# Optimization experiments

Measured on AMD Instinct MI355X. Metric: run time of the kernel, lower is better.

## Reference

```python
import jax, jax.numpy as jnp
import numpy as np
from jax import lax

# ---- model dims (match init_kwargs) ----
D = 2048        # hidden_size
HD = 128        # head_dim
HQ = 16         # num_q_heads (= expanded_num_heads)
HK = 8          # num_k_heads = num_v_heads
CONV = 4        # conv_size
CHUNK = 64      # chunk_size
NUM_ITER = 30   # chebyshev iterations
RIDGE = 0.02
EPS = 1e-6


def setup_inputs() -> dict:
    key = jax.random.key(0)
    ks = jax.random.split(key, 20)
    s = 0.02
    inp = {}
    inp['hidden_states'] = jax.random.normal(ks[0], (1, 1024, D), jnp.float32)
    inp['Wq'] = jax.random.normal(ks[1], (D, HQ * HD), jnp.float32) * s
    inp['Wk'] = jax.random.normal(ks[2], (D, HK * HD), jnp.float32) * s
    inp['Wv'] = jax.random.normal(ks[3], (D, HK * HD), jnp.float32) * s
    inp['conv_q'] = jax.random.normal(ks[4], (HQ * HD, CONV), jnp.float32) * 0.3
    inp['conv_k'] = jax.random.normal(ks[5], (HK * HD, CONV), jnp.float32) * 0.3
    inp['conv_v'] = jax.random.normal(ks[6], (HK * HD, CONV), jnp.float32) * 0.3
    inp['Wa'] = jax.random.normal(ks[7], (D, HQ), jnp.float32) * s
    # A_log = log(Uniform(0,16)) as in torch init
    inp['A_log'] = jnp.log(jax.random.uniform(ks[8], (HQ,), jnp.float32, 1e-3, 16.0))
    # dt_bias = inverse-softplus of dt ~ LogUniform(1e-3, 1e-1)
    dt = jnp.exp(jax.random.uniform(ks[9], (HQ,), jnp.float32) * (np.log(0.1) - np.log(0.001)) + np.log(0.001))
    dt = jnp.clip(dt, 1e-4, None)
    inp['dt_bias'] = dt + jnp.log(-jnp.expm1(-dt))
    inp['Wb'] = jax.random.normal(ks[10], (D, HQ), jnp.float32) * s
    inp['bb'] = jnp.zeros((HQ,), jnp.float32)
    inp['Walpha'] = jax.random.normal(ks[11], (D, HQ), jnp.float32) * s
    inp['balpha'] = jnp.zeros((HQ,), jnp.float32)
    inp['Wg'] = jax.random.normal(ks[12], (D, HQ * HD), jnp.float32) * s
    inp['norm_w'] = jnp.ones((HD,), jnp.float32)
    inp['Wo'] = jax.random.normal(ks[13], (HQ * HD, D), jnp.float32) * s
    return inp


def short_conv(x, w):
    # causal depthwise conv1d (kernel=CONV) + silu; x:[B,L,C], w:[C,K]
    K = w.shape[1]
    L = x.shape[1]
    xp = jnp.pad(x, ((0, 0), (K - 1, 0), (0, 0)))
    y = sum(xp[:, j:j + L, :] * w[:, j] for j in range(K))
    return jax.nn.silu(y)


def cheb_solve(A, b, lmin, lmax, num_iter):
    # Chebyshev semi-iteration for SPD A x = b, eigenvalue bounds [lmin, lmax].
    # A, b: [..., d, d]; lmin scalar; lmax: [..., 1, 1]
    theta = (lmax + lmin) / 2.0
    delta = (lmax - lmin) / 2.0
    sigma1 = theta / delta
    x = jnp.zeros_like(b)
    r = b
    rho = 1.0 / sigma1
    dvec = r / theta
    def body(carry, _):
        x, r, dvec, rho = carry
        x = x + dvec
        r = r - jnp.einsum('...de,...ef->...df', A, dvec)
        rho_n = 1.0 / (2.0 * sigma1 - rho)
        dvec = rho_n * rho * dvec + (2.0 * rho_n / delta) * r
        return (x, r, dvec, rho_n), None
    (x, _, _, _), _ = lax.scan(body, (x, r, dvec, rho), None, length=num_iter)
    return x


def reference(hidden_states, Wq, Wk, Wv, conv_q, conv_k, conv_v, Wa, A_log, dt_bias,
              Wb, bb, Walpha, balpha, Wg, norm_w, Wo):
    x = hidden_states
    B, L, _ = x.shape
    H, Hk, d, C = HQ, HK, HD, CHUNK
    Nc = L // C

    # projections + short causal convs with silu
    q = short_conv(x @ Wq, conv_q).reshape(B, L, H, d) * (d ** -0.5)  # gla rescale
    k = short_conv(x @ Wk, conv_k).reshape(B, L, Hk, d)
    v = short_conv(x @ Wv, conv_v).reshape(B, L, Hk, d)
    grp = H // Hk
    k = jnp.repeat(k, grp, axis=2)  # GQA expand: (h g) ordering
    v = jnp.repeat(v, grp, axis=2)

    # gates
    glog = -jnp.exp(A_log) * jax.nn.softplus(x @ Wa + dt_bias)   # [B,L,H], log forgetting gate <= 0
    beta = jax.nn.sigmoid(x @ Wb + bb)                           # [B,L,H]
    alpha = jax.nn.sigmoid(x @ Walpha + balpha)                  # [B,L,H]

    # chunk: [B,H,Nc,C,...]
    def ch(t):
        return t.reshape(B, Nc, C, H, -1).transpose(0, 3, 1, 2, 4)
    qc, kc, vc = ch(q), ch(k), ch(v)
    glc = glog.reshape(B, Nc, C, H).transpose(0, 3, 1, 2)   # [B,H,Nc,C]
    bc = beta.reshape(B, Nc, C, H).transpose(0, 3, 1, 2)

    cs = jnp.cumsum(glc, axis=-1)         # inclusive cumulative log-decay within chunk
    G = cs[..., -1]                        # total chunk decay [B,H,Nc]
    w_end = jnp.exp(G[..., None] - cs) * bc
    dHn = jnp.einsum('bhnc,bhncd,bhnce->bhnde', w_end, kc, kc)  # gram increment (forgetting_gate_kk)
    dBn = jnp.einsum('bhnc,bhncd,bhnce->bhnde', w_end, kc, vc)  # kv increment
    dg = jnp.exp(G)

    # inter-chunk state recurrence (scan over chunks)
    def step(carry, inp):
        Hs, Bs = carry
        g_n, dH_n, dB_n = inp
        out = (Hs, Bs)  # state at chunk START
        Hs = g_n[..., None, None] * Hs + dH_n
        Bs = g_n[..., None, None] * Bs + dB_n
        return (Hs, Bs), out
    init = (jnp.zeros((B, H, d, d), x.dtype), jnp.zeros((B, H, d, d), x.dtype))
    inputs = (dg.transpose(2, 0, 1), dHn.transpose(2, 0, 1, 3, 4), dBn.transpose(2, 0, 1, 3, 4))
    _, (H0, B0) = lax.scan(step, init, inputs)  # [Nc,B,H,d,d]

    # ridge-regularized Kalman solve per chunk via Chebyshev
    A = H0 + RIDGE * jnp.eye(d, dtype=x.dtype)
    lmax = jnp.trace(A, axis1=-2, axis2=-1)[..., None, None]  # trace >= lambda_max for SPD
    X = cheb_solve(A, B0, RIDGE, lmax, NUM_ITER)              # [Nc,B,H,d,d]
    Xc = X.transpose(1, 2, 0, 3, 4)                           # [B,H,Nc,d,d]

    # inter-chunk readout (through solved state)
    o_inter = jnp.exp(cs)[..., None] * jnp.einsum('bhncd,bhnde->bhnce', qc, Xc)
    # intra-chunk causal gated attention
    diff = cs[..., :, None] - cs[..., None, :]                # [B,H,Nc,C,C]
    mask = jnp.tril(jnp.ones((C, C), bool))
    dmat = jnp.exp(jnp.where(mask, diff, -1e30))
    scores = jnp.einsum('bhncd,bhnjd->bhncj', qc, kc) * dmat * bc[..., None, :]
    o_intra = jnp.einsum('bhncj,bhnjd->bhncd', scores, vc)

    o = (o_inter + o_intra).transpose(0, 2, 3, 1, 4).reshape(B, L, H, d)
    o = o + alpha[..., None] * v   # alpha connection (residual value path)

    # gated RMSNorm + output projection
    g_out = (x @ Wg).reshape(B, L, H, d)
    o = o * lax.rsqrt(jnp.mean(o * o, axis=-1, keepdims=True) + EPS) * norm_w
    o = o * jax.nn.silu(g_out)
    return o.reshape(B, L, H * d) @ Wo
```

## Files before the change

### kernel.cpp

```cpp
#include <hip/hip_runtime.h>
#include <math.h>


#define LSEQ 1024
#define DM   2048
#define NHQ  16
#define NHK  8
#define HDIM 128
#define NCH  16
#define CSZ  64

typedef __attribute__((ext_vector_type(8))) short short8;
typedef __attribute__((ext_vector_type(4))) float floatx4;

__device__ __forceinline__ unsigned short f2bf(float f) {
  unsigned int u = __float_as_uint(f);
  u += 0x7fffu + ((u >> 16) & 1u);
  return (unsigned short)(u >> 16);
}
__device__ __forceinline__ float bf2f(unsigned short u) {
  return __uint_as_float(((unsigned int)u) << 16);
}

__device__ __forceinline__ void gload16(const unsigned short* g,
                                        unsigned short* l) {
  __builtin_amdgcn_global_load_lds(
      (const __attribute__((address_space(1))) unsigned int*)g,
      (__attribute__((address_space(3))) unsigned int*)l, 16, 0, 0);
}

__device__ __forceinline__ void tcast_fat(
    const float* __restrict__ W, unsigned short* __restrict__ Wt,
    int K, int N, int bn, int bk, int tid, float* __restrict__ t) {
  int k0 = bk * 128, n0 = bn * 64;
#pragma unroll
  for (int i = 0; i < 8; ++i) {
    int u = tid + i * 256;
    int r = u >> 4, c4 = u & 15;
    float4 v = *(const float4*)(W + (size_t)(k0 + r) * N + n0 + c4 * 4);
    float* dst = t + r * 65 + c4 * 4;
    dst[0] = v.x; dst[1] = v.y; dst[2] = v.z; dst[3] = v.w;
  }
  __syncthreads();
#pragma unroll
  for (int i = 0; i < 4; ++i) {
    int u2 = tid + i * 256;
    int klow = u2 & 7, nlow = (u2 >> 3) & 7;
    int khigh = (u2 >> 6) & 1, nhigh = (u2 >> 7) & 7;
    int k8 = (klow + khigh * 8) * 8;
    int nn = nlow + nhigh * 8;
    unsigned short o8[8];
#pragma unroll
    for (int j = 0; j < 8; ++j) o8[j] = f2bf(t[(k8 + j) * 65 + nn]);
    *(uint4*)(Wt + (size_t)(n0 + nn) * K + k0 + k8) = *(uint4*)o8;
  }
}

__global__ __launch_bounds__(256) void prep_kernel(
    const float* __restrict__ x, const float* __restrict__ Wq,
    const float* __restrict__ Wk, const float* __restrict__ Wv,
    const float* __restrict__ Wg, unsigned short* __restrict__ xb16,
    unsigned short* __restrict__ WtAll,
    const float* __restrict__ Wa, const float* __restrict__ Wbeta,
    const float* __restrict__ Wal, const float* __restrict__ A_log,
    const float* __restrict__ dtb, const float* __restrict__ bbv,
    const float* __restrict__ balv, float* __restrict__ glog,
    float* __restrict__ beta, float* __restrict__ alpha) {
  __shared__ float smem[128 * 65];
  int b = blockIdx.x, tid = threadIdx.x;
  if (b < 1024) {
    float* xr = smem;
    float* part = smem + 2048;
    int ts = b;
    for (int i = tid; i < 512; i += 256)
      ((float4*)xr)[i] = ((const float4*)(x + (size_t)ts * 2048))[i];
    __syncthreads();
    int o = tid >> 2, p = tid & 3;
    float s = 0.f;
    if (o < 48) {
      const float* W = (o < 16) ? Wa : (o < 32) ? Wbeta : Wal;
      int h = o & 15;
      int k0 = p * 512;
      for (int k = k0; k < k0 + 512; ++k) s = fmaf(xr[k], W[k * 16 + h], s);
    }
    part[tid] = s;
    __syncthreads();
    if (o < 48 && p == 0) {
      float dot = part[tid] + part[tid + 1] + part[tid + 2] + part[tid + 3];
      int h = o & 15;
      if (o < 16) {
        float za = dot + dtb[h];
        float sp = fmaxf(za, 0.f) + log1pf(expf(-fabsf(za)));
        glog[ts * 16 + h] = -expf(A_log[h]) * sp;
      } else if (o < 32) {
        beta[ts * 16 + h] = 1.f / (1.f + expf(-(dot + bbv[h])));
      } else {
        alpha[ts * 16 + h] = 1.f / (1.f + expf(-(dot + balv[h])));
      }
    }
  } else if (b < 2560) {
    int r = b - 1024;
    if (r < 512) {
      tcast_fat(Wq, WtAll, 2048, 2048, r & 31, r >> 5, tid, smem);
    } else if (r < 768) {
      int q = r - 512;
      tcast_fat(Wk, WtAll + (size_t)2048 * 2048, 2048, 1024, q & 15, q >> 4,
                tid, smem);
    } else if (r < 1024) {
      int q = r - 768;
      tcast_fat(Wv, WtAll + (size_t)3072 * 2048, 2048, 1024, q & 15, q >> 4,
                tid, smem);
    } else {
      int q = r - 1024;
      tcast_fat(Wg, WtAll + (size_t)4096 * 2048, 2048, 2048, q & 31, q >> 5,
                tid, smem);
    }
  } else {
    int i0 = (b - 2560) * 1024 + tid;
#pragma unroll
    for (int i = 0; i < 4; ++i) {
      int idx = i0 + i * 256;
      float4 v = ((const float4*)x)[idx];
      ushort4 u;
      u.x = f2bf(v.x); u.y = f2bf(v.y); u.z = f2bf(v.z); u.w = f2bf(v.w);
      ((ushort4*)xb16)[idx] = u;
    }
  }
}

template <int BN>
__global__ __launch_bounds__(256) void gemm_lds(
    const unsigned short* __restrict__ A, const unsigned short* __restrict__ Bt,
    float* __restrict__ C, int M, int N, int K) {
  __shared__ unsigned short As[128 * 64];
  __shared__ unsigned short Bs[BN * 64];
  constexpr int NT = BN / 32;
  constexpr int BCH = BN / 32;
  int tid = threadIdx.x;
  int wave = tid >> 6, lane = tid & 63;
  int ln = lane & 15, hi = lane >> 4;
  int wm = wave & 1, wn = wave >> 1;
  int m0 = blockIdx.y * 128, n0 = blockIdx.x * BN;
  int lrow = lane >> 3, lcol = (lane & 7) * 8;

  floatx4 acc[4][NT];
#pragma unroll
  for (int mt = 0; mt < 4; ++mt)
#pragma unroll
    for (int nt = 0; nt < NT; ++nt) acc[mt][nt] = (floatx4)(0.f);

  for (int k0 = 0; k0 < K; k0 += 64) {
#pragma unroll
    for (int i = 0; i < 4; ++i) {
      int c = wave * 4 + i;
      gload16(A + (size_t)(m0 + c * 8 + lrow) * K + k0 + lcol, As + c * 512);
    }
#pragma unroll
    for (int i = 0; i < BCH; ++i) {
      int c = wave * BCH + i;
      gload16(Bt + (size_t)(n0 + c * 8 + lrow) * K + k0 + lcol, Bs + c * 512);
    }
    __syncthreads();
#pragma unroll
    for (int kb = 0; kb < 2; ++kb) {
      short8 a[4], b[NT];
#pragma unroll
      for (int mt = 0; mt < 4; ++mt)
        a[mt] = *(const short8*)(As + (wm * 64 + mt * 16 + ln) * 64 +
                                 kb * 32 + hi * 8);
#pragma unroll
      for (int nt = 0; nt < NT; ++nt)
        b[nt] = *(const short8*)(Bs + (wn * (BN / 2) + nt * 16 + ln) * 64 +
                                 kb * 32 + hi * 8);
#pragma unroll
      for (int mt = 0; mt < 4; ++mt)
#pragma unroll
        for (int nt = 0; nt < NT; ++nt)
          acc[mt][nt] = __builtin_amdgcn_mfma_f32_16x16x32_bf16(
              a[mt], b[nt], acc[mt][nt], 0, 0, 0);
    }
    __syncthreads();
  }
#pragma unroll
  for (int mt = 0; mt < 4; ++mt)
#pragma unroll
    for (int nt = 0; nt < NT; ++nt) {
      int col = n0 + wn * (BN / 2) + nt * 16 + ln;
      int rowb = m0 + wm * 64 + mt * 16 + hi * 4;
#pragma unroll
      for (int r = 0; r < 4; ++r)
        C[(size_t)(rowb + r) * N + col] = acc[mt][nt][r];
    }
}

__device__ __forceinline__ float conv_core(
    const float* __restrict__ xin, const float* __restrict__ w,
    int idx, int instride, int nch, float scale) {
  int t = idx / nch, ch = idx - t * nch;
  float acc = 0.f;
#pragma unroll
  for (int j = 0; j < 4; ++j) {
    int tt = t + j - 3;
    float xv = (tt >= 0) ? xin[(size_t)tt * instride + ch] : 0.f;
    acc = fmaf(xv, w[ch * 4 + j], acc);
  }
  return acc / (1.f + expf(-acc)) * scale;
}

__global__ __launch_bounds__(256) void conv_all(
    const float* __restrict__ xall, const float* __restrict__ convq,
    const float* __restrict__ convk, const float* __restrict__ convv,
    unsigned short* __restrict__ qs16, float* __restrict__ ks2,
    unsigned short* __restrict__ ks16, float* __restrict__ vs2,
    const float* __restrict__ glog, const float* __restrict__ beta,
    float* __restrict__ cs, float* __restrict__ wend) {
  int b = blockIdx.x, tid = threadIdx.x;
  if (b < 8192) {
    int idx = b * 256 + tid;
    qs16[idx] = f2bf(conv_core(xall, convq, idx, 6144, 2048,
                               0.08838834764831845f));
  } else if (b < 12288) {
    int idx = (b - 8192) * 256 + tid;
    float v = conv_core(xall + 2048, convk, idx, 6144, 1024, 1.0f);
    ks2[idx] = v;
    ks16[idx] = f2bf(v);
  } else if (b < 16384) {
    int idx = (b - 12288) * 256 + tid;
    vs2[idx] = conv_core(xall + 3072, convv, idx, 6144, 1024, 1.0f);
  } else {
    int idx = tid;
    int n = idx & 15;
    float acc = 0.f;
    for (int c = 0; c < CSZ; ++c) {
      acc += glog[(n * CSZ + c) * NHQ + (idx >> 4)];
      cs[idx * CSZ + c] = acc;
    }
    float G = acc;
    for (int c = 0; c < CSZ; ++c) {
      wend[idx * CSZ + c] =
          expf(G - cs[idx * CSZ + c]) * beta[(n * CSZ + c) * NHQ + (idx >> 4)];
    }
  }
}

__global__ __launch_bounds__(256) void dhb_kernel(
    const float* __restrict__ ks, const float* __restrict__ vs,
    const float* __restrict__ wend, float* __restrict__ dH,
    float* __restrict__ dB, unsigned short* __restrict__ vT16) {
  __shared__ uint4 smem4[4096];
  int bid = blockIdx.x;
  int tid = threadIdx.x;

  if (bid >= 256) {
    float* t = (float*)smem4;
    int b = bid - 256;
    size_t gbase = ((size_t)(b >> 3)) * 65536 + ((size_t)(b & 7)) * 128;
#pragma unroll
    for (int g = 0; g < 8; ++g) {
      int i = tid + g * 256;
      int c = i >> 5, e4 = i & 31;
      float4 v = *(const float4*)(vs + gbase + (size_t)c * 1024 + e4 * 4);
      t[c * 132 + e4 * 4 + 0] = v.x;
      t[c * 132 + e4 * 4 + 1] = v.y;
      t[c * 132 + e4 * 4 + 2] = v.z;
      t[c * 132 + e4 * 4 + 3] = v.w;
    }
    __syncthreads();
    int e = tid >> 1, half = tid & 1;
    size_t obase = ((size_t)b << 13) + (size_t)e * 64 + half * 32;
#pragma unroll
    for (int cc = 0; cc < 8; ++cc) {
      int c0 = half * 32 + cc * 4;
      ushort4 u;
      u.x = f2bf(t[(c0 + 0) * 132 + e]);
      u.y = f2bf(t[(c0 + 1) * 132 + e]);
      u.z = f2bf(t[(c0 + 2) * 132 + e]);
      u.w = f2bf(t[(c0 + 3) * 132 + e]);
      *(ushort4*)(vT16 + obase + cc * 4) = u;
    }
    return;
  }

  unsigned short (*skF)[8192] = (unsigned short (*)[8192])smem4;
  unsigned short (*svF)[8192] =
      (unsigned short (*)[8192])((unsigned short*)smem4 + 16384);
  int h = bid >> 4, n = bid & 15;
  int hk = h >> 1;

#pragma unroll
  for (int p = 0; p < 4; ++p) {
    int t2 = tid + p * 256;
    int c0 = (t2 >> 7) << 3;
    int e = t2 & 127;
    int base = ((e >> 4) * 2 + (c0 >> 5)) * 512 +
               ((c0 & 31) >> 3) * 128 + (e & 15) * 8;
    unsigned short kh[8], kl[8], vh[8], vl[8];
#pragma unroll
    for (int j = 0; j < 8; ++j) {
      int c = c0 + j;
      float s = sqrtf(wend[bid * 64 + c]);
      size_t g = (size_t)(n * 64 + c) * 1024 + hk * 128 + e;
      float kf = s * ks[g];
      float vf = s * vs[g];
      unsigned short khh = f2bf(kf);
      kh[j] = khh; kl[j] = f2bf(kf - bf2f(khh));
      unsigned short vhh = f2bf(vf);
      vh[j] = vhh; vl[j] = f2bf(vf - bf2f(vhh));
    }
    *(uint4*)(&skF[0][base]) = *(uint4*)kh;
    *(uint4*)(&skF[1][base]) = *(uint4*)kl;
    *(uint4*)(&svF[0][base]) = *(uint4*)vh;
    *(uint4*)(&svF[1][base]) = *(uint4*)vl;
  }
  __syncthreads();

  int w = tid >> 6, lane = tid & 63;
  int ln = lane & 15, hi = lane >> 4;

  short8 ah[2][2], al[2][2];
#pragma unroll
  for (int mti = 0; mti < 2; ++mti) {
    int mt = w * 2 + mti;
#pragma unroll
    for (int ct = 0; ct < 2; ++ct) {
      ah[mti][ct] = *(const short8*)(&skF[0][((mt * 2 + ct) * 64 + lane) * 8]);
      al[mti][ct] = *(const short8*)(&skF[1][((mt * 2 + ct) * 64 + lane) * 8]);
    }
  }

  size_t gb = (size_t)bid << 14;
#pragma unroll
  for (int which = 0; which < 2; ++which) {
    const unsigned short (*BF)[8192] = which ? svF : skF;
    float* outp = which ? dB : dH;
#pragma unroll
    for (int nt = 0; nt < 8; ++nt) {
      floatx4 a0 = (floatx4)(0.f), a1 = (floatx4)(0.f);
#pragma unroll
      for (int ct = 0; ct < 2; ++ct) {
        short8 bh = *(const short8*)(&BF[0][((nt * 2 + ct) * 64 + lane) * 8]);
        short8 bl = *(const short8*)(&BF[1][((nt * 2 + ct) * 64 + lane) * 8]);
        a0 = __builtin_amdgcn_mfma_f32_16x16x32_bf16(ah[0][ct], bh, a0, 0, 0, 0);
        a0 = __builtin_amdgcn_mfma_f32_16x16x32_bf16(ah[0][ct], bl, a0, 0, 0, 0);
        a0 = __builtin_amdgcn_mfma_f32_16x16x32_bf16(al[0][ct], bh, a0, 0, 0, 0);
        a1 = __builtin_amdgcn_mfma_f32_16x16x32_bf16(ah[1][ct], bh, a1, 0, 0, 0);
        a1 = __builtin_amdgcn_mfma_f32_16x16x32_bf16(ah[1][ct], bl, a1, 0, 0, 0);
        a1 = __builtin_amdgcn_mfma_f32_16x16x32_bf16(al[1][ct], bh, a1, 0, 0, 0);
      }
      int e = nt * 16 + ln;
#pragma unroll
      for (int rg = 0; rg < 4; ++rg) {
        int d0 = (w * 2 + 0) * 16 + hi * 4 + rg;
        int d1 = (w * 2 + 1) * 16 + hi * 4 + rg;
        outp[gb + (size_t)d0 * 128 + e] = a0[rg];
        outp[gb + (size_t)d1 * 128 + e] = a1[rg];
      }
    }
  }
}

__global__ __launch_bounds__(256) void scan_kernel(
    float* __restrict__ dH, float* __restrict__ dB,
    const float* __restrict__ cs) {
  int idx = blockIdx.x * 256 + threadIdx.x;
  int h = idx >> 14, de = idx & 16383;
  float Hs = 0.f, Bs = 0.f;
  bool diag = ((de % 129) == 0);
#pragma unroll 1
  for (int n = 0; n < NCH; ++n) {
    size_t off = ((size_t)(h * 16 + n) << 14) + de;
    float dh = dH[off], db = dB[off];
    dH[off] = diag ? (Hs + 0.02f) : Hs;
    dB[off] = Bs;
    float g = expf(cs[(h * 16 + n) * CSZ + (CSZ - 1)]);
    Hs = fmaf(g, Hs, dh);
    Bs = fmaf(g, Bs, db);
  }
}

__global__ __launch_bounds__(256) void afrag_kernel(
    float* __restrict__ Aall, float* __restrict__ traces) {
  int bid = blockIdx.x;
  float* Ag = Aall + ((size_t)bid << 14);
  __shared__ float As[16384];
  int tid = threadIdx.x;
  for (int i = tid; i < 4096; i += 256)
    ((float4*)As)[i] = ((const float4*)Ag)[i];
  __syncthreads();
  if (tid < 64) {
    float tv = As[tid * 129] + As[(tid + 64) * 129];
#pragma unroll
    for (int off = 32; off; off >>= 1) tv += __shfl_down(tv, off);
    if (tid == 0) traces[bid] = tv;
  }
  unsigned short* Ah = (unsigned short*)Ag;
  unsigned short* Al = Ah + 16384;
#pragma unroll
  for (int c8 = 0; c8 < 8; ++c8) {
    int s0 = tid * 64 + c8 * 8;
    int frag = s0 >> 9, mlane = (s0 >> 3) & 63;
    int m = ((frag >> 2) << 4) + (mlane & 15);
    int k = ((frag & 3) << 5) + ((mlane >> 4) << 3);
    unsigned short hi[8], lo[8];
#pragma unroll
    for (int j = 0; j < 8; ++j) {
      float a = As[m * 128 + k + j];
      unsigned short h = f2bf(a);
      hi[j] = h;
      lo[j] = f2bf(a - bf2f(h));
    }
    *(uint4*)(Ah + s0) = *(uint4*)hi;
    *(uint4*)(Al + s0) = *(uint4*)lo;
  }
}

__global__ __launch_bounds__(256, 4) void cheb_kernel(
    const unsigned short* __restrict__ Afrag, const float* __restrict__ traces,
    float* __restrict__ Ball) {
  int bid = blockIdx.x;
  int bm = bid & 255;
  int cb = bid >> 8;
  const unsigned short* __restrict__ Ah = Afrag + ((size_t)bm << 15);
  float* __restrict__ Bg = Ball + ((size_t)bm << 14);
  __shared__ unsigned short dT[2][2048];
  int tid = threadIdx.x;
  int w = tid >> 6, lane = tid & 63;
  int ln = lane & 15, q = lane >> 4;

  float lmax = traces[bm];
  const float lmin = 0.02f;
  float theta = 0.5f * (lmax + lmin);
  float delta = 0.5f * (lmax - lmin);
  float sigma1 = theta / delta;
  float rho = delta / theta;
  float invtheta = 1.f / theta;

  short8 afr[2][4][2];
#pragma unroll
  for (int mt = 0; mt < 2; ++mt)
#pragma unroll
    for (int kt = 0; kt < 4; ++kt) {
      int f = (w * 2 + mt) * 4 + kt;
      afr[mt][kt][0] = *(const short8*)(Ah + ((f * 64 + lane) << 3));
      afr[mt][kt][1] = *(const short8*)(Ah + 16384 + ((f * 64 + lane) << 3));
    }

  int wrB[2];
#pragma unroll
  for (int mt = 0; mt < 2; ++mt)
    wrB[mt] = w * 512 + (((mt * 2 + (q >> 1)) & 3) * 16 + ln) * 8 +
              ((q & 1) << 2);

  float xx[2][4], rr[2][4], dd[2][4];
#pragma unroll
  for (int mt = 0; mt < 2; ++mt) {
    ushort4 pack;
    unsigned short* pp = (unsigned short*)&pack;
#pragma unroll
    for (int rg = 0; rg < 4; ++rg) {
      float b = Bg[(w * 32 + mt * 16 + q * 4 + rg) * 128 + cb * 16 + ln];
      rr[mt][rg] = b;
      xx[mt][rg] = 0.f;
      unsigned short dq = f2bf(b * invtheta);
      dd[mt][rg] = bf2f(dq);
      pp[rg] = dq;
    }
    *(ushort4*)(&dT[0][wrB[mt]]) = pack;
  }
  __syncthreads();

#pragma unroll 1
  for (int it = 0; it < 30; ++it) {
    const unsigned short* dTr = dT[it & 1];
    unsigned short* dTw = dT[(it & 1) ^ 1];
    floatx4 a0 = (floatx4)(0.f), a1 = (floatx4)(0.f);
#pragma unroll
    for (int kt = 0; kt < 4; ++kt) {
      short8 df = *(const short8*)(dTr + kt * 512 + lane * 8);
      a0 = __builtin_amdgcn_mfma_f32_16x16x32_bf16(afr[0][kt][0], df, a0, 0, 0, 0);
      a0 = __builtin_amdgcn_mfma_f32_16x16x32_bf16(afr[0][kt][1], df, a0, 0, 0, 0);
      a1 = __builtin_amdgcn_mfma_f32_16x16x32_bf16(afr[1][kt][0], df, a1, 0, 0, 0);
      a1 = __builtin_amdgcn_mfma_f32_16x16x32_bf16(afr[1][kt][1], df, a1, 0, 0, 0);
    }
    float rho_n = 1.f / (2.f * sigma1 - rho);
    float c1s = rho_n * rho;
    float c2s = 2.f * rho_n / delta;
#pragma unroll
    for (int mt = 0; mt < 2; ++mt) {
      ushort4 pack;
      unsigned short* pp = (unsigned short*)&pack;
#pragma unroll
      for (int rg = 0; rg < 4; ++rg) {
        xx[mt][rg] += dd[mt][rg];
        rr[mt][rg] -= mt ? a1[rg] : a0[rg];
        float dn = fmaf(c1s, dd[mt][rg], c2s * rr[mt][rg]);
        unsigned short dq = f2bf(dn);
        dd[mt][rg] = bf2f(dq);
        pp[rg] = dq;
      }
      *(ushort4*)(&dTw[wrB[mt]]) = pack;
    }
    rho = rho_n;
    __syncthreads();
  }

  unsigned short* Xf = (unsigned short*)Bg;
#pragma unroll
  for (int mt = 0; mt < 2; ++mt) {
    ushort4 h4, l4;
    unsigned short* hp = (unsigned short*)&h4;
    unsigned short* lp = (unsigned short*)&l4;
#pragma unroll
    for (int rg = 0; rg < 4; ++rg) {
      float xv = xx[mt][rg];
      unsigned short h = f2bf(xv);
      hp[rg] = h;
      lp[rg] = f2bf(xv - bf2f(h));
    }
    int lhi = wrB[mt];
    int llo = lhi + 2048;
    *(ushort4*)(Xf + ((lhi >> 5) << 8) + (cb << 5) + (lhi & 31)) = h4;
    *(ushort4*)(Xf + ((llo >> 5) << 8) + (cb << 5) + (llo & 31)) = l4;
  }
}

__global__ __launch_bounds__(256) void attn_kernel(
    const unsigned short* __restrict__ q16, const unsigned short* __restrict__ k16,
    const unsigned short* __restrict__ vT16, const unsigned short* __restrict__ Xf,
    const float* __restrict__ vs, const float* __restrict__ cs,
    const float* __restrict__ beta, const float* __restrict__ alpha,
    float* __restrict__ o) {
  int bid = blockIdx.x;
  int h = bid >> 4, n = bid & 15;
  int hk = h >> 1;
  __shared__ unsigned short qb[64 * 136];
  __shared__ unsigned short kb[64 * 136];
  __shared__ unsigned short Sb[64 * 72];
  __shared__ float csL[64], ecsL[64], betaL[64], alphaL[64];
  int tid = threadIdx.x;
  int w = tid >> 6, lane = tid & 63;
  int ln = lane & 15, hi = lane >> 4;

  {
    size_t qgb = (((size_t)(n * 64)) * 16 + h) * 128;
    size_t kgb = (((size_t)(n * 64)) * 8 + hk) * 128;
#pragma unroll
    for (int g = 0; g < 4; ++g) {
      int i = tid + g * 256;
      int c = i >> 4, ch = i & 15;
      *(uint4*)(qb + c * 136 + ch * 8) =
          *(const uint4*)(q16 + qgb + (size_t)c * 2048 + ch * 8);
      *(uint4*)(kb + c * 136 + ch * 8) =
          *(const uint4*)(k16 + kgb + (size_t)c * 1024 + ch * 8);
    }
    if (tid < 64) {
      float cv = cs[bid * 64 + tid];
      csL[tid] = cv;
      ecsL[tid] = expf(cv);
      betaL[tid] = beta[(n * 64 + tid) * 16 + h];
      alphaL[tid] = alpha[(n * 64 + tid) * 16 + h];
    }
  }
  __syncthreads();

  short8 aq[4];
#pragma unroll
  for (int dt = 0; dt < 4; ++dt)
    aq[dt] = *(const short8*)(qb + (w * 16 + ln) * 136 + dt * 32 + hi * 8);

  const unsigned short* Xb = Xf + ((size_t)bid << 15);
  floatx4 acc[8];
#pragma unroll
  for (int et = 0; et < 8; ++et) {
    floatx4 a = (floatx4)(0.f);
#pragma unroll
    for (int dt = 0; dt < 4; ++dt) {
      int base = ((dt * 16 + (lane >> 2)) << 8) + (et << 5) + ((lane & 3) << 3);
      short8 xh = *(const short8*)(Xb + base);
      short8 xl = *(const short8*)(Xb + base + 16384);
      a = __builtin_amdgcn_mfma_f32_16x16x32_bf16(aq[dt], xh, a, 0, 0, 0);
      a = __builtin_amdgcn_mfma_f32_16x16x32_bf16(aq[dt], xl, a, 0, 0, 0);
    }
    acc[et] = a;
  }
#pragma unroll
  for (int et = 0; et < 8; ++et)
#pragma unroll
    for (int rg = 0; rg < 4; ++rg)
      acc[et][rg] *= ecsL[w * 16 + hi * 4 + rg];

#pragma unroll
  for (int jt = 0; jt < 4; ++jt) {
    if (jt <= w) {
      floatx4 s = (floatx4)(0.f);
#pragma unroll
      for (int dt = 0; dt < 4; ++dt) {
        short8 bk = *(const short8*)(kb + (jt * 16 + ln) * 136 + dt * 32 + hi * 8);
        s = __builtin_amdgcn_mfma_f32_16x16x32_bf16(aq[dt], bk, s, 0, 0, 0);
      }
      int j = jt * 16 + ln;
      float csj = csL[j], bj = betaL[j];
#pragma unroll
      for (int rg = 0; rg < 4; ++rg) {
        int c = w * 16 + hi * 4 + rg;
        float v = (j <= c) ? s[rg] * expf(csL[c] - csj) * bj : 0.f;
        Sb[c * 72 + j] = f2bf(v);
      }
    } else {
#pragma unroll
      for (int rg = 0; rg < 4; ++rg)
        Sb[(w * 16 + hi * 4 + rg) * 72 + jt * 16 + ln] = 0;
    }
  }

  const unsigned short* vTb = vT16 + ((size_t)(n * 8 + hk) << 13);
#pragma unroll
  for (int et = 0; et < 8; ++et) {
#pragma unroll
    for (int kt = 0; kt < 2; ++kt) {
      short8 as = *(const short8*)(Sb + (w * 16 + ln) * 72 + kt * 32 + hi * 8);
      short8 bv = *(const short8*)(vTb + (et * 16 + ln) * 64 + kt * 32 + hi * 8);
      acc[et] = __builtin_amdgcn_mfma_f32_16x16x32_bf16(as, bv, acc[et], 0, 0, 0);
    }
  }

#pragma unroll
  for (int et = 0; et < 8; ++et) {
#pragma unroll
    for (int rg = 0; rg < 4; ++rg) {
      int c = w * 16 + hi * 4 + rg, e = et * 16 + ln;
      size_t oaddr = (((size_t)(n * 64 + c)) * 16 + h) * 128 + e;
      size_t vaddr = (((size_t)(n * 64 + c)) * 8 + hk) * 128 + e;
      o[oaddr] = acc[et][rg] + alphaL[c] * vs[vaddr];
    }
  }
}

__global__ __launch_bounds__(256) void rmso_kernel(
    const float* __restrict__ o, const float* __restrict__ xall,
    const float* __restrict__ norm_w, unsigned short* __restrict__ onorm,
    const float* __restrict__ Wo, unsigned short* __restrict__ WtWo) {
  __shared__ float t[128 * 65];
  int b = blockIdx.x, tid = threadIdx.x;
  if (b < 512) {
    tcast_fat(Wo, WtWo, 2048, 2048, b & 31, b >> 5, tid, t);
  } else {
    int bb = b - 512;
    int wave = tid >> 6, lane = tid & 63;
    int row = bb * 4 + wave;
    size_t base = (size_t)row * HDIM;
    size_t gbase = (size_t)(row >> 4) * 6144 + 4096 + (size_t)(row & 15) * HDIM;
    float v0 = o[base + lane], v1 = o[base + lane + 64];
    float ss = fmaf(v0, v0, v1 * v1);
#pragma unroll
    for (int off = 32; off; off >>= 1) ss += __shfl_down(ss, off);
    ss = __shfl(ss, 0);
    float rinv = rsqrtf(ss * (1.f / 128.f) + 1e-6f);
    float g0 = xall[gbase + lane], g1 = xall[gbase + lane + 64];
    float s0 = g0 / (1.f + expf(-g0));
    float s1 = g1 / (1.f + expf(-g1));
    onorm[base + lane]      = f2bf(v0 * rinv * norm_w[lane] * s0);
    onorm[base + lane + 64] = f2bf(v1 * rinv * norm_w[lane + 64] * s1);
  }
}

extern "C" void kernel_launch(void* const* d_in, const int* in_sizes, int n_in,
                              void* d_out, int out_size, void* d_ws,
                              size_t ws_size, hipStream_t stream) {
  (void)in_sizes; (void)n_in; (void)out_size; (void)ws_size;
  const float* x      = (const float*)d_in[0];
  const float* Wq     = (const float*)d_in[1];
  const float* Wk     = (const float*)d_in[2];
  const float* Wv     = (const float*)d_in[3];
  const float* convq  = (const float*)d_in[4];
  const float* convk  = (const float*)d_in[5];
  const float* convv  = (const float*)d_in[6];
  const float* Wa     = (const float*)d_in[7];
  const float* A_log  = (const float*)d_in[8];
  const float* dtb    = (const float*)d_in[9];
  const float* Wb     = (const float*)d_in[10];
  const float* bbv    = (const float*)d_in[11];
  const float* Wal    = (const float*)d_in[12];
  const float* balv   = (const float*)d_in[13];
  const float* Wg     = (const float*)d_in[14];
  const float* norm_w = (const float*)d_in[15];
  const float* Wo     = (const float*)d_in[16];
  float* out = (float*)d_out;

  float* p = (float*)d_ws;
  float* xall  = p; p += 6291456;
  float* qslot = p; p += 2097152;
  float* ks2   = p; p += 1048576;
  float* vs2   = p; p += 1048576;
  float* ob    = p; p += 2097152;
  float* glog  = p; p += 16384;
  float* beta  = p; p += 16384;
  float* alpha = p; p += 16384;
  float* csb   = p; p += 16384;
  float* wend  = p; p += 16384;
  float* traces= p; p += 16384;
  float* dHn   = p; p += 4194304;
  float* dBn   = p; p += 4194304;
  unsigned short* xb16 = (unsigned short*)p; p += 1048576;

  unsigned short* qs16 = (unsigned short*)qslot;
  unsigned short* ks16 = qs16 + 2097152;
  unsigned short* vT16 = ks16 + 1048576;
  unsigned short* WtAll = (unsigned short*)dHn;
  unsigned short* WtWo  = (unsigned short*)ks2;
  unsigned short* onorm16 = xb16;

  dim3 blk(256);
  prep_kernel<<<3072, blk, 0, stream>>>(x, Wq, Wk, Wv, Wg, xb16, WtAll,
                                        Wa, Wb, Wal, A_log, dtb, bbv, balv,
                                        glog, beta, alpha);
  gemm_lds<128><<<dim3(48, 8), blk, 0, stream>>>(xb16, WtAll, xall,
                                                 1024, 6144, 2048);
  conv_all<<<16385, blk, 0, stream>>>(xall, convq, convk, convv,
                                      qs16, ks2, ks16, vs2,
                                      glog, beta, csb, wend);
  dhb_kernel<<<384, blk, 0, stream>>>(ks2, vs2, wend, dHn, dBn, vT16);
  scan_kernel<<<1024, blk, 0, stream>>>(dHn, dBn, csb);
  afrag_kernel<<<256, blk, 0, stream>>>(dHn, traces);
  cheb_kernel<<<2048, blk, 0, stream>>>((unsigned short*)dHn, traces, dBn);
  attn_kernel<<<256, blk, 0, stream>>>(qs16, ks16, vT16, (unsigned short*)dBn,
                                       vs2, csb, beta, alpha, ob);
  rmso_kernel<<<4608, blk, 0, stream>>>(ob, xall, norm_w, onorm16, Wo, WtWo);
  gemm_lds<64><<<dim3(32, 8), blk, 0, stream>>>(onorm16, WtWo, out,
                                                1024, 2048, 2048);
}
```

Measured before the change: 429.4 us.

## Retile GEMMs for more blocks, use packed bf16 convert in Chebyshev loop

New measurement: 415.4 us. 3.3% less time.

```diff
diff --git a/kernel.cpp b/kernel.cpp
--- a/kernel.cpp
+++ b/kernel.cpp
@@ -20,6 +20,12 @@
 }
 __device__ __forceinline__ float bf2f(unsigned short u) {
   return __uint_as_float(((unsigned int)u) << 16);
+}
+
+__device__ __forceinline__ unsigned int cvtpk(float a, float b) {
+  unsigned int r;
+  asm("v_cvt_pk_bf16_f32 %0, %1, %2" : "=v"(r) : "v"(a), "v"(b));
+  return r;
 }
 
 __device__ __forceinline__ void gload16(const unsigned short* g,
@@ -128,31 +134,33 @@
   }
 }
 
-template <int BN>
+template <int BM, int BN>
 __global__ __launch_bounds__(256) void gemm_lds(
     const unsigned short* __restrict__ A, const unsigned short* __restrict__ Bt,
     float* __restrict__ C, int M, int N, int K) {
-  __shared__ unsigned short As[128 * 64];
+  __shared__ unsigned short As[BM * 64];
   __shared__ unsigned short Bs[BN * 64];
+  constexpr int MT = BM / 32;
   constexpr int NT = BN / 32;
+  constexpr int ACH = BM / 32;
   constexpr int BCH = BN / 32;
   int tid = threadIdx.x;
   int wave = tid >> 6, lane = tid & 63;
   int ln = lane & 15, hi = lane >> 4;
   int wm = wave & 1, wn = wave >> 1;
-  int m0 = blockIdx.y * 128, n0 = blockIdx.x * BN;
+  int m0 = blockIdx.y * BM, n0 = blockIdx.x * BN;
   int lrow = lane >> 3, lcol = (lane & 7) * 8;
 
-  floatx4 acc[4][NT];
-#pragma unroll
-  for (int mt = 0; mt < 4; ++mt)
+  floatx4 acc[MT][NT];
+#pragma unroll
+  for (int mt = 0; mt < MT; ++mt)
 #pragma unroll
     for (int nt = 0; nt < NT; ++nt) acc[mt][nt] = (floatx4)(0.f);
 
   for (int k0 = 0; k0 < K; k0 += 64) {
 #pragma unroll
-    for (int i = 0; i < 4; ++i) {
-      int c = wave * 4 + i;
+    for (int i = 0; i < ACH; ++i) {
+      int c = wave * ACH + i;
       gload16(A + (size_t)(m0 + c * 8 + lrow) * K + k0 + lcol, As + c * 512);
     }
 #pragma unroll
@@ -163,17 +171,17 @@
     __syncthreads();
 #pragma unroll
     for (int kb = 0; kb < 2; ++kb) {
-      short8 a[4], b[NT];
-#pragma unroll
-      for (int mt = 0; mt < 4; ++mt)
-        a[mt] = *(const short8*)(As + (wm * 64 + mt * 16 + ln) * 64 +
+      short8 a[MT], b[NT];
+#pragma unroll
+      for (int mt = 0; mt < MT; ++mt)
+        a[mt] = *(const short8*)(As + (wm * (BM / 2) + mt * 16 + ln) * 64 +
                                  kb * 32 + hi * 8);
 #pragma unroll
       for (int nt = 0; nt < NT; ++nt)
         b[nt] = *(const short8*)(Bs + (wn * (BN / 2) + nt * 16 + ln) * 64 +
                                  kb * 32 + hi * 8);
 #pragma unroll
-      for (int mt = 0; mt < 4; ++mt)
+      for (int mt = 0; mt < MT; ++mt)
 #pragma unroll
         for (int nt = 0; nt < NT; ++nt)
           acc[mt][nt] = __builtin_amdgcn_mfma_f32_16x16x32_bf16(
@@ -182,11 +190,11 @@
     __syncthreads();
   }
 #pragma unroll
-  for (int mt = 0; mt < 4; ++mt)
+  for (int mt = 0; mt < MT; ++mt)
 #pragma unroll
     for (int nt = 0; nt < NT; ++nt) {
       int col = n0 + wn * (BN / 2) + nt * 16 + ln;
-      int rowb = m0 + wm * 64 + mt * 16 + hi * 4;
+      int rowb = m0 + wm * (BM / 2) + mt * 16 + hi * 4;
 #pragma unroll
       for (int r = 0; r < 4; ++r)
         C[(size_t)(rowb + r) * N + col] = acc[mt][nt][r];
@@ -414,7 +422,7 @@
   }
 }
 
-__global__ __launch_bounds__(256, 4) void cheb_kernel(
+__global__ __launch_bounds__(256, 2) void cheb_kernel(
     const unsigned short* __restrict__ Afrag, const float* __restrict__ traces,
     float* __restrict__ Ball) {
   int bid = blockIdx.x;
@@ -454,18 +462,21 @@
   float xx[2][4], rr[2][4], dd[2][4];
 #pragma unroll
   for (int mt = 0; mt < 2; ++mt) {
-    ushort4 pack;
-    unsigned short* pp = (unsigned short*)&pack;
 #pragma unroll
     for (int rg = 0; rg < 4; ++rg) {
       float b = Bg[(w * 32 + mt * 16 + q * 4 + rg) * 128 + cb * 16 + ln];
       rr[mt][rg] = b;
       xx[mt][rg] = 0.f;
-      unsigned short dq = f2bf(b * invtheta);
-      dd[mt][rg] = bf2f(dq);
-      pp[rg] = dq;
-    }
-    *(ushort4*)(&dT[0][wrB[mt]]) = pack;
+      dd[mt][rg] = b * invtheta;
+    }
+    unsigned int p01 = cvtpk(dd[mt][0], dd[mt][1]);
+    unsigned int p23 = cvtpk(dd[mt][2], dd[mt][3]);
+    dd[mt][0] = __uint_as_float(p01 << 16);
+    dd[mt][1] = __uint_as_float(p01 & 0xffff0000u);
+    dd[mt][2] = __uint_as_float(p23 << 16);
+    dd[mt][3] = __uint_as_float(p23 & 0xffff0000u);
+    uint2 pk; pk.x = p01; pk.y = p23;
+    *(uint2*)(&dT[0][wrB[mt]]) = pk;
   }
   __syncthreads();
 
@@ -487,18 +498,21 @@
     float c2s = 2.f * rho_n / delta;
 #pragma unroll
     for (int mt = 0; mt < 2; ++mt) {
-      ushort4 pack;
-      unsigned short* pp = (unsigned short*)&pack;
+      float dn[4];
 #pragma unroll
       for (int rg = 0; rg < 4; ++rg) {
         xx[mt][rg] += dd[mt][rg];
         rr[mt][rg] -= mt ? a1[rg] : a0[rg];
-        float dn = fmaf(c1s, dd[mt][rg], c2s * rr[mt][rg]);
-        unsigned short dq = f2bf(dn);
-        dd[mt][rg] = bf2f(dq);
-        pp[rg] = dq;
+        dn[rg] = fmaf(c1s, dd[mt][rg], c2s * rr[mt][rg]);
       }
-      *(ushort4*)(&dTw[wrB[mt]]) = pack;
+      unsigned int p01 = cvtpk(dn[0], dn[1]);
+      unsigned int p23 = cvtpk(dn[2], dn[3]);
+      dd[mt][0] = __uint_as_float(p01 << 16);
+      dd[mt][1] = __uint_as_float(p01 & 0xffff0000u);
+      dd[mt][2] = __uint_as_float(p23 << 16);
+      dd[mt][3] = __uint_as_float(p23 & 0xffff0000u);
+      uint2 pk; pk.x = p01; pk.y = p23;
+      *(uint2*)(&dTw[wrB[mt]]) = pk;
     }
     rho = rho_n;
     __syncthreads();
@@ -714,8 +728,8 @@
   prep_kernel<<<3072, blk, 0, stream>>>(x, Wq, Wk, Wv, Wg, xb16, WtAll,
                                         Wa, Wb, Wal, A_log, dtb, bbv, balv,
                                         glog, beta, alpha);
-  gemm_lds<128><<<dim3(48, 8), blk, 0, stream>>>(xb16, WtAll, xall,
-                                                 1024, 6144, 2048);
+  gemm_lds<128, 64><<<dim3(96, 8), blk, 0, stream>>>(xb16, WtAll, xall,
+                                                     1024, 6144, 2048);
   conv_all<<<16385, blk, 0, stream>>>(xall, convq, convk, convv,
                                       qs16, ks2, ks16, vs2,
                                       glog, beta, csb, wend);
@@ -726,6 +740,6 @@
   attn_kernel<<<256, blk, 0, stream>>>(qs16, ks16, vT16, (unsigned short*)dBn,
                                        vs2, csb, beta, alpha, ob);
   rmso_kernel<<<4608, blk, 0, stream>>>(ob, xall, norm_w, onorm16, Wo, WtWo);
-  gemm_lds<64><<<dim3(32, 8), blk, 0, stream>>>(onorm16, WtWo, out,
-                                                1024, 2048, 2048);
-}
+  gemm_lds<64, 64><<<dim3(32, 16), blk, 0, stream>>>(onorm16, WtWo, out,
+                                                     1024, 2048, 2048);
+}
```
